# Optimization experiments

Measured on AMD Instinct MI355X. Metric: run time of the kernel, lower is better.

Reference implementation:

```python
import jax, jax.numpy as jnp
import numpy as np

EPS = 1e-09
NUM_ITERS = 3

def squash_axis2(s):
    # Faithful to CapsuleLayer.squash: reduces over dim=2 of the (5-D) torch
    # tensor; here s is [B, 1, J, V] and dim=2 is the num_units axis J.
    mag_sq = jnp.sum(s * s, axis=2, keepdims=True)
    mag = jnp.sqrt(mag_sq + EPS)
    return mag_sq / (1.0 + mag_sq) * (s / mag)

def setup_inputs() -> dict:
    key = jax.random.key(0)
    k1, k2 = jax.random.split(key)
    B, I, J, D, V = 64, 2048, 32, 128, 32
    x = jax.random.normal(k1, (B, I, D), dtype=jnp.float32)
    # W stored as [I, J, D, V] (torch param is [1, I, J, unit_size, vec_len])
    W = jax.random.normal(k2, (I, J, D, V), dtype=jnp.float32)
    return {"x": x, "W": W}

def reference(x, W):
    B, I, D = x.shape
    J, V = W.shape[1], W.shape[3]
    # u_hat[b,i,j,v] = sum_d W[i,j,d,v] * x[b,i,d]  (torch: W^T @ x per capsule)
    u_hat = jnp.einsum('ijdv,bid->bijv', W, x)  # [B, I, J, V]
    u_hat_sg = jax.lax.stop_gradient(u_hat)
    b_ij = jnp.zeros((B, I, J), dtype=x.dtype)
    v_j = None
    for it in range(NUM_ITERS):
        c_ij = jax.nn.softmax(b_ij, axis=1)  # softmax over num_caps_i (dim=1)
        uh = u_hat if it == NUM_ITERS - 1 else u_hat_sg
        s_j = jnp.sum(c_ij[..., None] * uh, axis=1, keepdims=True)  # [B,1,J,V]
        v_j = squash_axis2(s_j)  # [B,1,J,V] (squash reduces over J, as in source)
        if it < NUM_ITERS - 1:
            # agreement: <u_hat_i, v_j> -> [B,I,J], mean over batch, broadcast-add
            agree = jnp.einsum('bijv,bjv->bij', u_hat_sg, v_j[:, 0])
            b_ij = b_ij + jnp.mean(agree, axis=0, keepdims=True)
    return v_j[:, 0]  # squeeze -> [B, J, V]
```

## Files before the change

### kernel.cpp

```cpp
#include <hip/hip_runtime.h>
#include <math.h>

#define NI 2048
#define NJ 32
#define ND 128
#define NV 32
#define NB 64
#define NCH 64

typedef _Float16 f16x8 __attribute__((ext_vector_type(8)));
typedef float f32x4 __attribute__((ext_vector_type(4)));

__device__ __forceinline__ unsigned short f2h(float f) {
  _Float16 h = (_Float16)f;
  return __builtin_bit_cast(unsigned short, h);
}
__device__ __forceinline__ float h2f(unsigned short u) {
  return (float)__builtin_bit_cast(_Float16, u);
}

#define LOADKS(dst, wp, ks)                                                    \
  {                                                                            \
    _Pragma("unroll") for (int mt = 0; mt < 2; ++mt) {                         \
      const float* ap =                                                        \
          (wp) + (size_t)((ks) * 32 + lg * 8) * NV + mt * 16 + li;             \
      _Pragma("unroll") for (int e = 0; e < 8; ++e)                            \
          dst[mt * 8 + e] = ap[(size_t)e * NV];                                \
    }                                                                          \
  }

__global__ __launch_bounds__(256, 3) void k_uhat(
    const float* __restrict__ x, const float* __restrict__ W,
    unsigned short* __restrict__ uhat) {
  const int i = blockIdx.x;
  const int tid = threadIdx.x;
  const int wave = tid >> 6;
  const int lane = tid & 63;
  __shared__ unsigned short xs[64][136];

  {
    const int b = tid >> 2;
    const int d0 = (tid & 3) * 32;
    const float* xp = x + ((size_t)b * NI + i) * ND + d0;
#pragma unroll
    for (int c2 = 0; c2 < 8; ++c2) {
      f32x4 v = *(const f32x4*)(xp + 4 * c2);
      ushort4 h;
      h.x = f2h(v.x); h.y = f2h(v.y); h.z = f2h(v.z); h.w = f2h(v.w);
      *(ushort4*)&xs[b][d0 + 4 * c2] = h;
    }
  }
  __syncthreads();

  const int li = lane & 15;
  const int lg = lane >> 4;

  f16x8 xfrag[4][4];
#pragma unroll
  for (int nt = 0; nt < 4; ++nt)
#pragma unroll
    for (int ks = 0; ks < 4; ++ks)
      xfrag[nt][ks] = *(const f16x8*)&xs[nt * 16 + li][ks * 32 + lg * 8];

  const float* wp0 = W + ((size_t)i * NJ + wave * 8) * (ND * NV);
  float raw[2][16];
  LOADKS(raw[0], wp0, 0)

#pragma unroll 1
  for (int jj = 0; jj < 8; ++jj) {
    const int j = wave * 8 + jj;
    const float* wp = wp0 + (size_t)jj * (ND * NV);
    f32x4 acc[2][4];
#pragma unroll
    for (int mt = 0; mt < 2; ++mt)
#pragma unroll
      for (int nt = 0; nt < 4; ++nt)
        acc[mt][nt] = (f32x4){0.f, 0.f, 0.f, 0.f};

#pragma unroll
    for (int ks = 0; ks < 4; ++ks) {
      const int cur = ks & 1;
      const int nxt = cur ^ 1;
      if (ks < 3) {
        LOADKS(raw[nxt], wp, ks + 1)
      } else {
        const int jn = (jj + 1) & 7;
        const float* wpn = wp0 + (size_t)jn * (ND * NV);
        LOADKS(raw[nxt], wpn, 0)
      }
      f16x8 wfrag[2];
#pragma unroll
      for (int mt = 0; mt < 2; ++mt) {
        f16x8 af;
#pragma unroll
        for (int e = 0; e < 8; ++e) af[e] = (_Float16)raw[cur][mt * 8 + e];
        wfrag[mt] = af;
      }
#pragma unroll
      for (int mt = 0; mt < 2; ++mt)
#pragma unroll
        for (int nt = 0; nt < 4; ++nt)
          acc[mt][nt] = __builtin_amdgcn_mfma_f32_16x16x32_f16(
              wfrag[mt], xfrag[nt][ks], acc[mt][nt], 0, 0, 0);
    }

    unsigned short* up = uhat + ((size_t)j * NI + i) * (NB * NV);
#pragma unroll
    for (int mt = 0; mt < 2; ++mt)
#pragma unroll
      for (int nt = 0; nt < 4; ++nt) {
        const int b = nt * 16 + li;
        const int v0 = mt * 16 + lg * 4;
        ushort4 h4;
        h4.x = f2h(acc[mt][nt][0]);
        h4.y = f2h(acc[mt][nt][1]);
        h4.z = f2h(acc[mt][nt][2]);
        h4.w = f2h(acc[mt][nt][3]);
        *(ushort4*)(up + (size_t)b * NV + v0) = h4;
      }
  }
}

__global__ __launch_bounds__(256) void k_pass0(
    const unsigned short* __restrict__ uhat, float* __restrict__ spart) {
  const int j = blockIdx.x & 31;
  const int ch = blockIdx.x >> 5;
  const int tid = threadIdx.x;
  const int f0 = tid * 8;
  float acc[8] = {0, 0, 0, 0, 0, 0, 0, 0};
  const int i0 = ch * 32;
  const unsigned short* ubase = uhat + ((size_t)j * NI + i0) * (NB * NV) + f0;
#pragma unroll 4
  for (int ii = 0; ii < 32; ++ii) {
    const uint4 q = *(const uint4*)(ubase + (size_t)ii * (NB * NV));
    acc[0] += h2f((unsigned short)(q.x & 0xffff));
    acc[1] += h2f((unsigned short)(q.x >> 16));
    acc[2] += h2f((unsigned short)(q.y & 0xffff));
    acc[3] += h2f((unsigned short)(q.y >> 16));
    acc[4] += h2f((unsigned short)(q.z & 0xffff));
    acc[5] += h2f((unsigned short)(q.z >> 16));
    acc[6] += h2f((unsigned short)(q.w & 0xffff));
    acc[7] += h2f((unsigned short)(q.w >> 16));
  }
  const int b = f0 >> 5;
  const int v0 = f0 & 31;
  float* sp = spart + (size_t)ch * (NB * NJ * NV) + (size_t)b * (NJ * NV) + j * NV + v0;
  *(f32x4*)sp = (f32x4){acc[0], acc[1], acc[2], acc[3]};
  *(f32x4*)(sp + 4) = (f32x4){acc[4], acc[5], acc[6], acc[7]};
}

__global__ __launch_bounds__(256) void k_route(
    const unsigned short* __restrict__ uhat, const float* __restrict__ vprev,
    const float* __restrict__ bin, float* __restrict__ bout,
    float* __restrict__ spart, float* __restrict__ Zpart) {
  const int j = blockIdx.x & 31;
  const int ch = blockIdx.x >> 5;
  const int tid = threadIdx.x;
  const int wave = tid >> 6;
  const int lane = tid & 63;
  const int f0 = tid * 8;
  const int b = f0 >> 5;
  const int v0 = f0 & 31;
  __shared__ float red[2][4];

  const float* vp = vprev + (size_t)b * (NJ * NV) + j * NV + v0;
  const f32x4 vva = *(const f32x4*)vp;
  const f32x4 vvb = *(const f32x4*)(vp + 4);

  float acc[8] = {0, 0, 0, 0, 0, 0, 0, 0};
  float zacc = 0.0f;
  const int i0 = ch * 32;
  const float* binj = bin ? (bin + (size_t)j * NI) : nullptr;
  float* boutj = bout + (size_t)j * NI;
  const unsigned short* ubase = uhat + ((size_t)j * NI + i0) * (NB * NV) + f0;

#pragma unroll 2
  for (int ii = 0; ii < 32; ++ii) {
    const int i = i0 + ii;
    const float bprev = binj ? binj[i] : 0.0f;
    const uint4 q = *(const uint4*)(ubase + (size_t)ii * (NB * NV));
    float h[8];
    h[0] = h2f((unsigned short)(q.x & 0xffff));
    h[1] = h2f((unsigned short)(q.x >> 16));
    h[2] = h2f((unsigned short)(q.y & 0xffff));
    h[3] = h2f((unsigned short)(q.y >> 16));
    h[4] = h2f((unsigned short)(q.z & 0xffff));
    h[5] = h2f((unsigned short)(q.z >> 16));
    h[6] = h2f((unsigned short)(q.w & 0xffff));
    h[7] = h2f((unsigned short)(q.w >> 16));
    float dp = h[0] * vva.x + h[1] * vva.y + h[2] * vva.z + h[3] * vva.w +
               h[4] * vvb.x + h[5] * vvb.y + h[6] * vvb.z + h[7] * vvb.w;
#pragma unroll
    for (int off = 32; off > 0; off >>= 1) dp += __shfl_xor(dp, off);
    const int par = ii & 1;
    if (lane == 0) red[par][wave] = dp;
    __syncthreads();
    const float agree = red[par][0] + red[par][1] + red[par][2] + red[par][3];
    const float bnew = bprev + agree * (1.0f / 64.0f);
    const float w = __expf(bnew);
    if (tid == 0) boutj[i] = bnew;
#pragma unroll
    for (int e = 0; e < 8; ++e) acc[e] = fmaf(w, h[e], acc[e]);
    zacc += w;
  }
  if (tid == 0) Zpart[ch * NJ + j] = zacc;
  float* sp = spart + (size_t)ch * (NB * NJ * NV) + (size_t)b * (NJ * NV) + j * NV + v0;
  *(f32x4*)sp = (f32x4){acc[0], acc[1], acc[2], acc[3]};
  *(f32x4*)(sp + 4) = (f32x4){acc[4], acc[5], acc[6], acc[7]};
}

__global__ __launch_bounds__(1024) void k_squash(
    const float* __restrict__ spart, const float* __restrict__ Zpart,
    const float scale0, float* __restrict__ vout) {
  const int b = blockIdx.x;
  const int tid = threadIdx.x;
  const int j = tid >> 5;
  const int v = tid & 31;
  __shared__ float zs[NJ];
  if (Zpart != nullptr) {
    if (tid < NJ) {
      float z = 0.0f;
#pragma unroll 8
      for (int ch = 0; ch < NCH; ++ch) z += Zpart[ch * NJ + tid];
      zs[tid] = 1.0f / z;
    }
    __syncthreads();
  }
  const float scale = (Zpart != nullptr) ? zs[j] : scale0;
  float s = 0.0f;
#pragma unroll 8
  for (int ch = 0; ch < NCH; ++ch)
    s += spart[(size_t)ch * (NB * NJ * NV) + (size_t)b * (NJ * NV) + tid];
  s *= scale;
  __shared__ float sq[NJ][NV + 1];
  sq[j][v] = s * s;
  __syncthreads();
#pragma unroll
  for (int off = 16; off > 0; off >>= 1) {
    if (j < off) sq[j][v] += sq[j + off][v];
    __syncthreads();
  }
  const float msq = sq[0][v];
  const float f = msq / ((1.0f + msq) * sqrtf(msq + 1e-9f));
  vout[(size_t)b * (NJ * NV) + tid] = f * s;
}

extern "C" void kernel_launch(void* const* d_in, const int* in_sizes, int n_in,
                              void* d_out, int out_size, void* d_ws, size_t ws_size,
                              hipStream_t stream) {
  (void)in_sizes; (void)n_in; (void)out_size; (void)ws_size;
  const float* x = (const float*)d_in[0];
  const float* W = (const float*)d_in[1];
  float* out = (float*)d_out;

  char* ws = (char*)d_ws;
  const size_t UHAT_BYTES = (size_t)NI * NJ * NB * NV * 2;
  unsigned short* uhat = (unsigned short*)ws;
  float* bbuf = (float*)(ws + UHAT_BYTES);
  float* spart = bbuf + (size_t)NI * NJ;
  float* vt = spart + (size_t)NCH * NB * NJ * NV;
  float* Zpart = vt + (size_t)NB * NJ * NV;

  k_uhat<<<dim3(NI), dim3(256), 0, stream>>>(x, W, uhat);

  k_pass0<<<dim3(NCH * NJ), dim3(256), 0, stream>>>(uhat, spart);
  k_squash<<<dim3(NB), dim3(1024), 0, stream>>>(spart, nullptr, 1.0f / NI, vt);

  k_route<<<dim3(NCH * NJ), dim3(256), 0, stream>>>(uhat, vt, nullptr, bbuf, spart, Zpart);
  k_squash<<<dim3(NB), dim3(1024), 0, stream>>>(spart, Zpart, 0.0f, vt);

  k_route<<<dim3(NCH * NJ), dim3(256), 0, stream>>>(uhat, vt, bbuf, bbuf, spart, Zpart);
  k_squash<<<dim3(NB), dim3(1024), 0, stream>>>(spart, Zpart, 0.0f, out);
}
```

Before: 468.5 us.

## Stage W slabs into LDS via direct global-to-LDS loads with XOR swizzle

Replaces per-lane strided scalar global loads of W (8 scalar loads per mt at stride NV) with 16-byte global_load_lds transfers into a per-wave double-buffered LDS slab. A manual vmcnt wait and sched_barrier provide the pipelining, and an XOR swizzle on the column index avoids bank conflicts when fragments are read back. The goal is fewer, wider, coalesced memory transactions for the W stream that dominates the u_hat kernel. In exchange it adds 32KB of LDS per block, which may lower occupancy below the 3-block launch bound, and it relies on a hand-written waitcnt whose correctness depends on there being no other outstanding loads.

```diff
diff --git a/kernel.cpp b/kernel.cpp
--- a/kernel.cpp
+++ b/kernel.cpp
@@ -19,15 +19,11 @@
   return (float)__builtin_bit_cast(_Float16, u);
 }
 
-#define LOADKS(dst, wp, ks)                                                    \
-  {                                                                            \
-    _Pragma("unroll") for (int mt = 0; mt < 2; ++mt) {                         \
-      const float* ap =                                                        \
-          (wp) + (size_t)((ks) * 32 + lg * 8) * NV + mt * 16 + li;             \
-      _Pragma("unroll") for (int e = 0; e < 8; ++e)                            \
-          dst[mt * 8 + e] = ap[(size_t)e * NV];                                \
-    }                                                                          \
-  }
+__device__ __forceinline__ void gload_lds16(const float* g, float* l) {
+  __builtin_amdgcn_global_load_lds(
+      (const __attribute__((address_space(1))) void*)g,
+      (__attribute__((address_space(3))) void*)l, 16, 0, 0);
+}
 
 __global__ __launch_bounds__(256, 3) void k_uhat(
     const float* __restrict__ x, const float* __restrict__ W,
@@ -37,6 +33,7 @@
   const int wave = tid >> 6;
   const int lane = tid & 63;
   __shared__ unsigned short xs[64][136];
+  __shared__ float wslab[4][2][1024];
 
   {
     const int b = tid >> 2;
@@ -62,9 +59,24 @@
     for (int ks = 0; ks < 4; ++ks)
       xfrag[nt][ks] = *(const f16x8*)&xs[nt * 16 + li][ks * 32 + lg * 8];
 
+  const int lane_base0 = (lane >> 3) * 32 + ((lane & 7) * 4);
+  const int lane_base1 = (lane >> 3) * 32 + (((lane & 7) * 4) ^ 16);
+
+#define STAGE_SLAB(buf, srcbase)                                               \
+  {                                                                            \
+    gload_lds16((srcbase) + 0 * 256 + lane_base0, &wslab[wave][buf][0 * 256]); \
+    gload_lds16((srcbase) + 1 * 256 + lane_base1, &wslab[wave][buf][1 * 256]); \
+    gload_lds16((srcbase) + 2 * 256 + lane_base0, &wslab[wave][buf][2 * 256]); \
+    gload_lds16((srcbase) + 3 * 256 + lane_base1, &wslab[wave][buf][3 * 256]); \
+  }
+
   const float* wp0 = W + ((size_t)i * NJ + wave * 8) * (ND * NV);
-  float raw[2][16];
-  LOADKS(raw[0], wp0, 0)
+  int cur = 0;
+  STAGE_SLAB(0, wp0)
+
+  const int vv0 = (0 * 16 + li) ^ ((lg & 1) << 4);
+  const int vv1 = (1 * 16 + li) ^ ((lg & 1) << 4);
+  const int rb = lg * 256;
 
 #pragma unroll 1
   for (int jj = 0; jj < 8; ++jj) {
@@ -79,22 +91,18 @@
 
 #pragma unroll
     for (int ks = 0; ks < 4; ++ks) {
-      const int cur = ks & 1;
-      const int nxt = cur ^ 1;
-      if (ks < 3) {
-        LOADKS(raw[nxt], wp, ks + 1)
-      } else {
-        const int jn = (jj + 1) & 7;
-        const float* wpn = wp0 + (size_t)jn * (ND * NV);
-        LOADKS(raw[nxt], wpn, 0)
-      }
+      const float* nsrc = (ks < 3)
+                              ? (wp + (size_t)(ks + 1) * 1024)
+                              : (wp0 + (size_t)((jj + 1) & 7) * (ND * NV));
+      STAGE_SLAB(cur ^ 1, nsrc)
+      asm volatile("s_waitcnt vmcnt(4)" ::: "memory");
+      __builtin_amdgcn_sched_barrier(0);
+
       f16x8 wfrag[2];
 #pragma unroll
-      for (int mt = 0; mt < 2; ++mt) {
-        f16x8 af;
-#pragma unroll
-        for (int e = 0; e < 8; ++e) af[e] = (_Float16)raw[cur][mt * 8 + e];
-        wfrag[mt] = af;
+      for (int e = 0; e < 8; ++e) {
+        wfrag[0][e] = (_Float16)wslab[wave][cur][rb + e * 32 + vv0];
+        wfrag[1][e] = (_Float16)wslab[wave][cur][rb + e * 32 + vv1];
       }
 #pragma unroll
       for (int mt = 0; mt < 2; ++mt)
@@ -102,6 +110,7 @@
         for (int nt = 0; nt < 4; ++nt)
           acc[mt][nt] = __builtin_amdgcn_mfma_f32_16x16x32_f16(
               wfrag[mt], xfrag[nt][ks], acc[mt][nt], 0, 0, 0);
+      cur ^= 1;
     }
 
     unsigned short* up = uhat + ((size_t)j * NI + i) * (NB * NV);
@@ -119,6 +128,7 @@
         *(ushort4*)(up + (size_t)b * NV + v0) = h4;
       }
   }
+#undef STAGE_SLAB
 }
 
 __global__ __launch_bounds__(256) void k_pass0(
```

After: 471.7 us. Within noise of the previous version (+0.7%).

## Fuse routing iterations into one cooperative persistent kernel with grid syncs

Applied to the files above, without the earlier changes.

Replaces the six separate pass/route/squash launches with a single cooperative kernel that loops over tasks per block and uses grid-wide synchronization between phases. Squash is rewritten for 256-thread blocks with a simpler column reduction. The intent is to remove kernel launch gaps and tail effects between small dependent kernels, at the cost of grid.sync overhead and occupancy limits from the cooperative launch. A fallback path keeps the multi-kernel sequence if cooperative launch fails.

```diff
diff --git a/kernel.cpp b/kernel.cpp
--- a/kernel.cpp
+++ b/kernel.cpp
@@ -1,5 +1,8 @@
 #include <hip/hip_runtime.h>
+#include <hip/hip_cooperative_groups.h>
 #include <math.h>
+
+namespace cg = cooperative_groups;
 
 #define NI 2048
 #define NJ 32
@@ -121,10 +124,11 @@
   }
 }
 
-__global__ __launch_bounds__(256) void k_pass0(
-    const unsigned short* __restrict__ uhat, float* __restrict__ spart) {
-  const int j = blockIdx.x & 31;
-  const int ch = blockIdx.x >> 5;
+__device__ __forceinline__ void pass0_body(
+    int task, const unsigned short* __restrict__ uhat,
+    float* __restrict__ spart) {
+  const int j = task & 31;
+  const int ch = task >> 5;
   const int tid = threadIdx.x;
   const int f0 = tid * 8;
   float acc[8] = {0, 0, 0, 0, 0, 0, 0, 0};
@@ -149,19 +153,19 @@
   *(f32x4*)(sp + 4) = (f32x4){acc[4], acc[5], acc[6], acc[7]};
 }
 
-__global__ __launch_bounds__(256) void k_route(
-    const unsigned short* __restrict__ uhat, const float* __restrict__ vprev,
-    const float* __restrict__ bin, float* __restrict__ bout,
-    float* __restrict__ spart, float* __restrict__ Zpart) {
-  const int j = blockIdx.x & 31;
-  const int ch = blockIdx.x >> 5;
+__device__ __forceinline__ void route_body(
+    int task, const unsigned short* __restrict__ uhat,
+    const float* __restrict__ vprev, const float* __restrict__ bin,
+    float* __restrict__ bout, float* __restrict__ spart,
+    float* __restrict__ Zpart, float (&red)[2][4]) {
+  const int j = task & 31;
+  const int ch = task >> 5;
   const int tid = threadIdx.x;
   const int wave = tid >> 6;
   const int lane = tid & 63;
   const int f0 = tid * 8;
   const int b = f0 >> 5;
   const int v0 = f0 & 31;
-  __shared__ float red[2][4];
 
   const float* vp = vprev + (size_t)b * (NJ * NV) + j * NV + v0;
   const f32x4 vva = *(const f32x4*)vp;
@@ -209,40 +213,100 @@
   *(f32x4*)(sp + 4) = (f32x4){acc[4], acc[5], acc[6], acc[7]};
 }
 
-__global__ __launch_bounds__(1024) void k_squash(
-    const float* __restrict__ spart, const float* __restrict__ Zpart,
-    const float scale0, float* __restrict__ vout) {
-  const int b = blockIdx.x;
+__device__ __forceinline__ void squash_body(
+    int b, const float* __restrict__ spart, const float* __restrict__ Zpart,
+    float scale0, float* __restrict__ vout, float (&sq)[NJ][NV + 1],
+    float (&zinv)[NJ], float (&msq)[NV]) {
   const int tid = threadIdx.x;
-  const int j = tid >> 5;
-  const int v = tid & 31;
-  __shared__ float zs[NJ];
   if (Zpart != nullptr) {
     if (tid < NJ) {
       float z = 0.0f;
 #pragma unroll 8
       for (int ch = 0; ch < NCH; ++ch) z += Zpart[ch * NJ + tid];
-      zs[tid] = 1.0f / z;
+      zinv[tid] = 1.0f / z;
     }
     __syncthreads();
   }
-  const float scale = (Zpart != nullptr) ? zs[j] : scale0;
-  float s = 0.0f;
+  float sv[4];
+#pragma unroll
+  for (int k = 0; k < 4; ++k) {
+    const int slot = tid + 256 * k;
+    const int j = slot >> 5;
+    float s = 0.0f;
 #pragma unroll 8
-  for (int ch = 0; ch < NCH; ++ch)
-    s += spart[(size_t)ch * (NB * NJ * NV) + (size_t)b * (NJ * NV) + tid];
-  s *= scale;
+    for (int ch = 0; ch < NCH; ++ch)
+      s += spart[(size_t)ch * (NB * NJ * NV) + (size_t)b * (NJ * NV) + slot];
+    s *= (Zpart != nullptr) ? zinv[j] : scale0;
+    sv[k] = s;
+    sq[j][slot & 31] = s * s;
+  }
+  __syncthreads();
+  if (tid < NV) {
+    float m = 0.0f;
+#pragma unroll
+    for (int j = 0; j < NJ; ++j) m += sq[j][tid];
+    msq[tid] = m;
+  }
+  __syncthreads();
+#pragma unroll
+  for (int k = 0; k < 4; ++k) {
+    const int slot = tid + 256 * k;
+    const float m = msq[slot & 31];
+    const float f = m / ((1.0f + m) * sqrtf(m + 1e-9f));
+    vout[(size_t)b * (NJ * NV) + slot] = f * sv[k];
+  }
+  __syncthreads();
+}
+
+__global__ __launch_bounds__(256, 4) void k_routing(
+    const unsigned short* __restrict__ uhat, float* __restrict__ bbuf,
+    float* __restrict__ spart, float* __restrict__ Zpart,
+    float* __restrict__ vt, float* __restrict__ out) {
+  cg::grid_group grid = cg::this_grid();
+  __shared__ float red[2][4];
   __shared__ float sq[NJ][NV + 1];
-  sq[j][v] = s * s;
-  __syncthreads();
-#pragma unroll
-  for (int off = 16; off > 0; off >>= 1) {
-    if (j < off) sq[j][v] += sq[j + off][v];
-    __syncthreads();
-  }
-  const float msq = sq[0][v];
-  const float f = msq / ((1.0f + msq) * sqrtf(msq + 1e-9f));
-  vout[(size_t)b * (NJ * NV) + tid] = f * s;
+  __shared__ float zinv[NJ];
+  __shared__ float msq[NV];
+
+  for (int t = blockIdx.x; t < NCH * NJ; t += gridDim.x)
+    pass0_body(t, uhat, spart);
+  grid.sync();
+  for (int b = blockIdx.x; b < NB; b += gridDim.x)
+    squash_body(b, spart, nullptr, 1.0f / NI, vt, sq, zinv, msq);
+  grid.sync();
+  for (int t = blockIdx.x; t < NCH * NJ; t += gridDim.x)
+    route_body(t, uhat, vt, nullptr, bbuf, spart, Zpart, red);
+  grid.sync();
+  for (int b = blockIdx.x; b < NB; b += gridDim.x)
+    squash_body(b, spart, Zpart, 0.0f, vt, sq, zinv, msq);
+  grid.sync();
+  for (int t = blockIdx.x; t < NCH * NJ; t += gridDim.x)
+    route_body(t, uhat, vt, bbuf, bbuf, spart, Zpart, red);
+  grid.sync();
+  for (int b = blockIdx.x; b < NB; b += gridDim.x)
+    squash_body(b, spart, Zpart, 0.0f, out, sq, zinv, msq);
+}
+
+__global__ __launch_bounds__(256) void k_pass0(
+    const unsigned short* __restrict__ uhat, float* __restrict__ spart) {
+  pass0_body(blockIdx.x, uhat, spart);
+}
+
+__global__ __launch_bounds__(256) void k_route(
+    const unsigned short* __restrict__ uhat, const float* __restrict__ vprev,
+    const float* __restrict__ bin, float* __restrict__ bout,
+    float* __restrict__ spart, float* __restrict__ Zpart) {
+  __shared__ float red[2][4];
+  route_body(blockIdx.x, uhat, vprev, bin, bout, spart, Zpart, red);
+}
+
+__global__ __launch_bounds__(256) void k_squash(
+    const float* __restrict__ spart, const float* __restrict__ Zpart,
+    const float scale0, float* __restrict__ vout) {
+  __shared__ float sq[NJ][NV + 1];
+  __shared__ float zinv[NJ];
+  __shared__ float msq[NV];
+  squash_body(blockIdx.x, spart, Zpart, scale0, vout, sq, zinv, msq);
 }
 
 extern "C" void kernel_launch(void* const* d_in, const int* in_sizes, int n_in,
@@ -251,7 +315,7 @@
   (void)in_sizes; (void)n_in; (void)out_size; (void)ws_size;
   const float* x = (const float*)d_in[0];
   const float* W = (const float*)d_in[1];
-  float* out = (float*)d_out;
+  float* outp = (float*)d_out;
 
   char* ws = (char*)d_ws;
   const size_t UHAT_BYTES = (size_t)NI * NJ * NB * NV * 2;
@@ -263,12 +327,26 @@
 
   k_uhat<<<dim3(NI), dim3(256), 0, stream>>>(x, W, uhat);
 
-  k_pass0<<<dim3(NCH * NJ), dim3(256), 0, stream>>>(uhat, spart);
-  k_squash<<<dim3(NB), dim3(1024), 0, stream>>>(spart, nullptr, 1.0f / NI, vt);
-
-  k_route<<<dim3(NCH * NJ), dim3(256), 0, stream>>>(uhat, vt, nullptr, bbuf, spart, Zpart);
-  k_squash<<<dim3(NB), dim3(1024), 0, stream>>>(spart, Zpart, 0.0f, vt);
-
-  k_route<<<dim3(NCH * NJ), dim3(256), 0, stream>>>(uhat, vt, bbuf, bbuf, spart, Zpart);
-  k_squash<<<dim3(NB), dim3(1024), 0, stream>>>(spart, Zpart, 0.0f, out);
-}
+  int maxBlk = 0;
+  hipError_t qe = hipOccupancyMaxActiveBlocksPerMultiprocessor(
+      &maxBlk, (const void*)k_routing, 256, 0);
+  hipError_t le = hipErrorUnknown;
+  if (qe == hipSuccess && maxBlk >= 1) {
+    int grid = maxBlk * 256;
+    if (grid > NCH * NJ) grid = NCH * NJ;
+    void* args[] = {(void*)&uhat, (void*)&bbuf, (void*)&spart,
+                    (void*)&Zpart, (void*)&vt, (void*)&outp};
+    le = hipLaunchCooperativeKernel((const void*)k_routing, dim3(grid),
+                                    dim3(256), args, 0, stream);
+  }
+  if (le != hipSuccess) {
+    k_pass0<<<dim3(NCH * NJ), dim3(256), 0, stream>>>(uhat, spart);
+    k_squash<<<dim3(NB), dim3(256), 0, stream>>>(spart, nullptr, 1.0f / NI, vt);
+    k_route<<<dim3(NCH * NJ), dim3(256), 0, stream>>>(uhat, vt, nullptr, bbuf,
+                                                      spart, Zpart);
+    k_squash<<<dim3(NB), dim3(256), 0, stream>>>(spart, Zpart, 0.0f, vt);
+    k_route<<<dim3(NCH * NJ), dim3(256), 0, stream>>>(uhat, vt, bbuf, bbuf,
+                                                      spart, Zpart);
+    k_squash<<<dim3(NB), dim3(256), 0, stream>>>(spart, Zpart, 0.0f, outp);
+  }
+}
```

Result: slower. 1.013 ms (+116.2%).
